# Performance work log

Measured on AMD Instinct MI355X. Metric: run time of the kernel, lower is better.

## Reference

```python
import jax, jax.numpy as jnp
import numpy as np

A1, A2 = 16, 16            # block tile sizes (arr_size1, arr_size2)
G = 1000                   # graph_size (max node index + 1)
EG = 16000                 # number of graph edges (avg degree 16)
SIZE1 = G * A1             # input feature length  (16000)
SIZE2 = G * A2             # output feature length (16000)
NNZ = EG * A1 * A2         # expanded COO entries  (4,096,000)
B = 32                     # batch


def _expand_indices(t0, t1, a1, a2):
    """Vectorized adjust_indices: edge (t0,t1) -> tile of (row,col) pairs.
    row = t0*a2 + j, col = t1*a1 + i  for all i in [a1), j in [a2)."""
    e = t0.shape[0]
    j = np.arange(a2)
    i = np.arange(a1)
    rows = np.broadcast_to(t0[:, None, None] * a2 + j[None, None, :], (e, a1, a2)).reshape(-1)
    cols = np.broadcast_to(t1[:, None, None] * a1 + i[None, :, None], (e, a1, a2)).reshape(-1)
    return rows.astype(np.int32), cols.astype(np.int32)


def setup_inputs() -> dict:
    key = jax.random.key(0)
    ks = jax.random.split(key, 6)
    rng = np.random.default_rng(0)
    t0 = rng.integers(0, G, EG)
    t1 = rng.integers(0, G, EG)
    rows_np, cols_np = _expand_indices(t0, t1, A1, A2)
    # original init: uniform(-1/len(indices), 1/len(indices)) with len([2,nnz])==2 -> U(-0.5, 0.5)
    return {
        "x": jax.random.normal(ks[0], (B, SIZE1, 1), dtype=jnp.float32),
        "weight_mean": jax.random.uniform(ks[1], (NNZ,), jnp.float32, -0.5, 0.5),
        "weight_log_var": jnp.zeros((NNZ,), jnp.float32),
        "b_mean": jax.random.uniform(ks[2], (SIZE2,), jnp.float32, -0.5, 0.5),
        "b_log_var": jnp.zeros((SIZE2,), jnp.float32),
        "eps_w": jax.random.normal(ks[3], (NNZ,), dtype=jnp.float32),
        "eps_b": jax.random.normal(ks[4], (SIZE2,), dtype=jnp.float32),
        "rows": jnp.asarray(rows_np),
        "cols": jnp.asarray(cols_np),
    }


def reference(x, weight_mean, weight_log_var, b_mean, b_log_var, eps_w, eps_b, rows, cols):
    # reparameterization sample of sparse weight values
    values = eps_w * jnp.exp(weight_log_var) + weight_mean          # [NNZ]
    # COO spmm: out[b, r, k] += values[e] * x[b, c, k] for each (r, c) = (rows[e], cols[e])
    contrib = values[None, :, None] * x[:, cols, :]                 # [B, NNZ, 1]
    out = jnp.zeros((x.shape[0], SIZE2, x.shape[2]), x.dtype).at[:, rows, :].add(contrib)
    # reparameterized bias, broadcast over batch
    b = eps_b * jnp.exp(b_log_var) + b_mean                         # [SIZE2]
    out = out + b[None, :, None]
    # kl is explicitly zeroed in the source right before return
    return (out, jnp.asarray(0.0, dtype=x.dtype))
```

## Files before the change

kernel.cpp:

```cpp
#include <hip/hip_runtime.h>

#define EG   16000
#define BB   32
#define SIZE 16000

__global__ __launch_bounds__(256) void init_out_kernel(
    const float* __restrict__ bm, const float* __restrict__ blv,
    const float* __restrict__ eb, float* __restrict__ out)
{
    int r = blockIdx.x * 256 + threadIdx.x;
    int b = blockIdx.y;
    if (r < SIZE) {
        float bias = eb[r] * __expf(blv[r]) + bm[r];
        out[b * SIZE + r] = bias;
    }
    if (blockIdx.x == 0 && blockIdx.y == 0 && threadIdx.x == 0)
        out[BB * SIZE] = 0.0f;
}

__global__ __launch_bounds__(256) void edge_kernel(
    const float* __restrict__ wm, const float* __restrict__ wlv,
    const float* __restrict__ ew, const float* __restrict__ x,
    const int* __restrict__ rows, const int* __restrict__ cols,
    float* __restrict__ out)
{
    __shared__ float vt[256];
    __shared__ float xs[512];

    int e    = blockIdx.x;
    int tid  = threadIdx.x;
    int base = e << 8;

    int t0 = rows[base] >> 4;
    int t1 = cols[base] >> 4;

    vt[tid] = ew[base + tid] * __expf(wlv[base + tid]) + wm[base + tid];

    int j  = tid & 15;
    int b0 = tid >> 4;
    int xb = t1 << 4;
    xs[tid]       = x[ b0        * SIZE + xb + j];
    xs[tid + 256] = x[(b0 + 16)  * SIZE + xb + j];
    __syncthreads();

    float acc0 = 0.f, acc1 = 0.f;
    #pragma unroll
    for (int i = 0; i < 16; ++i) {
        float vv = vt[(i << 4) + j];
        acc0 += vv * xs[((b0)      << 4) + i];
        acc1 += vv * xs[((b0 + 16) << 4) + i];
    }

    int r = (t0 << 4) + j;
    unsafeAtomicAdd(&out[ b0       * SIZE + r], acc0);
    unsafeAtomicAdd(&out[(b0 + 16) * SIZE + r], acc1);
}

extern "C" void kernel_launch(void* const* d_in, const int* in_sizes, int n_in,
                              void* d_out, int out_size, void* d_ws, size_t ws_size,
                              hipStream_t stream) {
    const float* x   = (const float*)d_in[0];
    const float* wm  = (const float*)d_in[1];
    const float* wlv = (const float*)d_in[2];
    const float* bm  = (const float*)d_in[3];
    const float* blv = (const float*)d_in[4];
    const float* ew  = (const float*)d_in[5];
    const float* eb  = (const float*)d_in[6];
    const int* rows  = (const int*)d_in[7];
    const int* cols  = (const int*)d_in[8];
    float* out = (float*)d_out;

    init_out_kernel<<<dim3((SIZE + 255) / 256, BB), 256, 0, stream>>>(bm, blv, eb, out);
    edge_kernel<<<EG, 256, 0, stream>>>(wm, wlv, ew, x, rows, cols, out);
}
```

Before: 137.0 us.

## Process four edges per block with vectorized nontemporal weight loads

Each block now handles four edge tiles instead of one. Weights are read as float4 with nontemporal loads and stored transposed in shared memory so the dot products use vector LDS reads. Launch overhead per block and per-edge index loads are amortized across the four edges, and the atomics per thread rise to eight. The host pointer shuffle is confusing but ends up passing the same arguments as before.

Result: slower. 147.8 us (+7.8%).

```diff
diff --git a/kernel.cpp b/kernel.cpp
--- a/kernel.cpp
+++ b/kernel.cpp
@@ -3,6 +3,8 @@
 #define EG   16000
 #define BB   32
 #define SIZE 16000
+
+typedef float f32x4 __attribute__((ext_vector_type(4)));
 
 __global__ __launch_bounds__(256) void init_out_kernel(
     const float* __restrict__ bm, const float* __restrict__ blv,
@@ -24,36 +26,83 @@
     const int* __restrict__ rows, const int* __restrict__ cols,
     float* __restrict__ out)
 {
-    __shared__ float vt[256];
-    __shared__ float xs[512];
+    __shared__ float vtT[1024];
+    __shared__ float xs[2048];
+    __shared__ int   st0[4];
+    __shared__ int   st1[4];
 
-    int e    = blockIdx.x;
-    int tid  = threadIdx.x;
-    int base = e << 8;
+    int tid = threadIdx.x;
+    int grp = blockIdx.x;
+    int E   = grp << 2;
 
-    int t0 = rows[base] >> 4;
-    int t1 = cols[base] >> 4;
+    if (tid < 8) {
+        int k = tid & 3;
+        if (tid < 4) st1[k] = cols[(long)(E + k) << 8] >> 4;
+        else         st0[k] = rows[(long)(E + k) << 8] >> 4;
+    }
 
-    vt[tid] = ew[base + tid] * __expf(wlv[base + tid]) + wm[base + tid];
+    const f32x4* wm4  = (const f32x4*)wm;
+    const f32x4* wlv4 = (const f32x4*)wlv;
+    const f32x4* ew4  = (const f32x4*)ew;
+    int qi = (grp << 8) + tid;
+    f32x4 m4 = __builtin_nontemporal_load(&wm4[qi]);
+    f32x4 l4 = __builtin_nontemporal_load(&wlv4[qi]);
+    f32x4 e4 = __builtin_nontemporal_load(&ew4[qi]);
+    f32x4 v4;
+    v4.x = e4.x * __expf(l4.x) + m4.x;
+    v4.y = e4.y * __expf(l4.y) + m4.y;
+    v4.z = e4.z * __expf(l4.z) + m4.z;
+    v4.w = e4.w * __expf(l4.w) + m4.w;
+    {
+        int k  = tid >> 6;
+        int i  = (tid >> 2) & 15;
+        int j0 = (tid & 3) << 2;
+        int b  = (k << 8) + i;
+        vtT[b + (j0    ) * 16] = v4.x;
+        vtT[b + (j0 + 1) * 16] = v4.y;
+        vtT[b + (j0 + 2) * 16] = v4.z;
+        vtT[b + (j0 + 3) * 16] = v4.w;
+    }
+    __syncthreads();
+
+    const f32x4* x4 = (const f32x4*)x;
+    f32x4* xs4 = (f32x4*)xs;
+    #pragma unroll
+    for (int h = 0; h < 2; ++h) {
+        int q   = tid + (h << 8);
+        int k   = q >> 7;
+        int rem = q & 127;
+        int b   = rem >> 2;
+        int i4  = rem & 3;
+        xs4[(k << 7) + (b << 2) + i4] =
+            x4[b * (SIZE / 4) + (st1[k] << 2) + i4];
+    }
+    __syncthreads();
 
     int j  = tid & 15;
     int b0 = tid >> 4;
-    int xb = t1 << 4;
-    xs[tid]       = x[ b0        * SIZE + xb + j];
-    xs[tid + 256] = x[(b0 + 16)  * SIZE + xb + j];
-    __syncthreads();
-
-    float acc0 = 0.f, acc1 = 0.f;
+    const f32x4* vtT4 = (const f32x4*)vtT;
+    float acc0[4], acc1[4];
     #pragma unroll
-    for (int i = 0; i < 16; ++i) {
-        float vv = vt[(i << 4) + j];
-        acc0 += vv * xs[((b0)      << 4) + i];
-        acc1 += vv * xs[((b0 + 16) << 4) + i];
+    for (int k = 0; k < 4; ++k) {
+        float a0 = 0.f, a1 = 0.f;
+        #pragma unroll
+        for (int q = 0; q < 4; ++q) {
+            f32x4 w  = vtT4[(k << 6) + (j << 2) + q];
+            f32x4 xa = xs4[(k << 7) + (b0 << 2) + q];
+            f32x4 xb = xs4[(k << 7) + ((b0 + 16) << 2) + q];
+            a0 += w.x * xa.x + w.y * xa.y + w.z * xa.z + w.w * xa.w;
+            a1 += w.x * xb.x + w.y * xb.y + w.z * xb.z + w.w * xb.w;
+        }
+        acc0[k] = a0; acc1[k] = a1;
     }
 
-    int r = (t0 << 4) + j;
-    unsafeAtomicAdd(&out[ b0       * SIZE + r], acc0);
-    unsafeAtomicAdd(&out[(b0 + 16) * SIZE + r], acc1);
+    #pragma unroll
+    for (int k = 0; k < 4; ++k) {
+        int r = (st0[k] << 4) + j;
+        unsafeAtomicAdd(&out[ b0       * SIZE + r], acc0[k]);
+        unsafeAtomicAdd(&out[(b0 + 16) * SIZE + r], acc1[k]);
+    }
 }
 
 extern "C" void kernel_launch(void* const* d_in, const int* in_sizes, int n_in,
@@ -64,12 +113,16 @@
     const float* wlv = (const float*)d_in[2];
     const float* bm  = (const float*)d_in[3];
     const float* blv = (const float*)d_in[4];
-    const float* ew  = (const float*)d_in[5];
-    const float* eb  = (const float*)d_in[6];
-    const int* rows  = (const int*)d_in[7];
-    const int* cols  = (const int*)d_in[8];
+    const float* eb  = (const float*)d_in[5];
+    const int* rows  = (const int*)d_in[6];
+    const int* cols  = (const int*)d_in[7];
+    (void)eb; (void)rows; (void)cols;
+    const float* ew_  = (const float*)d_in[5];
+    const float* eb_  = (const float*)d_in[6];
+    const int* rows_  = (const int*)d_in[7];
+    const int* cols_  = (const int*)d_in[8];
     float* out = (float*)d_out;
 
-    init_out_kernel<<<dim3((SIZE + 255) / 256, BB), 256, 0, stream>>>(bm, blv, eb, out);
-    edge_kernel<<<EG, 256, 0, stream>>>(wm, wlv, ew, x, rows, cols, out);
+    init_out_kernel<<<dim3((SIZE + 255) / 256, BB), 256, 0, stream>>>(bm, blv, eb_, out);
+    edge_kernel<<<EG / 4, 256, 0, stream>>>(wm, wlv, ew_, x, rows_, cols_, out);
 }
```

## Bucket edges by destination node and reduce per node without atomics

Applied to the files above, without the earlier changes.

Adds a bucketing pass that groups edges by destination tile row, then launches one block per output node. Each block accumulates all its incoming edge tiles with double-buffered vectorized loads and writes the result with the fused bias. This removes the global atomic adds and the separate output init kernel, at the cost of an extra memset and bucket pass, a fixed per-node capacity of 64 edges, and possible load imbalance across nodes.

Result: no change. 135.0 us (-1.5%).

```diff
diff --git a/kernel.cpp b/kernel.cpp
--- a/kernel.cpp
+++ b/kernel.cpp
@@ -1,59 +1,143 @@
 #include <hip/hip_runtime.h>
 
 #define EG   16000
+#define NG   1000
 #define BB   32
 #define SIZE 16000
+#define CAP  64
 
-__global__ __launch_bounds__(256) void init_out_kernel(
-    const float* __restrict__ bm, const float* __restrict__ blv,
-    const float* __restrict__ eb, float* __restrict__ out)
+typedef float f32x4 __attribute__((ext_vector_type(4)));
+
+__global__ __launch_bounds__(256) void bucket_kernel(
+    const int* __restrict__ rows, const int* __restrict__ cols,
+    int* __restrict__ cnt, int* __restrict__ bucket)
 {
-    int r = blockIdx.x * 256 + threadIdx.x;
-    int b = blockIdx.y;
-    if (r < SIZE) {
-        float bias = eb[r] * __expf(blv[r]) + bm[r];
-        out[b * SIZE + r] = bias;
+    int e = blockIdx.x * 256 + threadIdx.x;
+    if (e < EG) {
+        int t0 = rows[(long)e << 8] >> 4;
+        int t1 = cols[(long)e << 8] >> 4;
+        int pos = atomicAdd(&cnt[t0], 1);
+        if (pos < CAP) bucket[t0 * CAP + pos] = (e << 10) | t1;
     }
-    if (blockIdx.x == 0 && blockIdx.y == 0 && threadIdx.x == 0)
-        out[BB * SIZE] = 0.0f;
 }
 
-__global__ __launch_bounds__(256) void edge_kernel(
+__global__ __launch_bounds__(256) void spmm_kernel(
     const float* __restrict__ wm, const float* __restrict__ wlv,
     const float* __restrict__ ew, const float* __restrict__ x,
-    const int* __restrict__ rows, const int* __restrict__ cols,
+    const float* __restrict__ bm, const float* __restrict__ blv,
+    const float* __restrict__ eb,
+    const int* __restrict__ cnt, const int* __restrict__ bucket,
     float* __restrict__ out)
 {
-    __shared__ float vt[256];
-    __shared__ float xs[512];
+    __shared__ f32x4 vt[2][4][64];
+    __shared__ f32x4 xs[2][4][160];
+    __shared__ int   sl[CAP];
 
-    int e    = blockIdx.x;
+    int g    = blockIdx.x;
     int tid  = threadIdx.x;
-    int base = e << 8;
+    int wave = tid >> 6;
+    int lane = tid & 63;
+    int jg   = lane & 3;
+    int cb2  = lane >> 2;
 
-    int t0 = rows[base] >> 4;
-    int t1 = cols[base] >> 4;
-
-    vt[tid] = ew[base + tid] * __expf(wlv[base + tid]) + wm[base + tid];
-
-    int j  = tid & 15;
-    int b0 = tid >> 4;
-    int xb = t1 << 4;
-    xs[tid]       = x[ b0        * SIZE + xb + j];
-    xs[tid + 256] = x[(b0 + 16)  * SIZE + xb + j];
+    int n = cnt[g]; n = n < CAP ? n : CAP;
+    if (tid < n) sl[tid] = bucket[g * CAP + tid];
     __syncthreads();
 
-    float acc0 = 0.f, acc1 = 0.f;
-    #pragma unroll
-    for (int i = 0; i < 16; ++i) {
-        float vv = vt[(i << 4) + j];
-        acc0 += vv * xs[((b0)      << 4) + i];
-        acc1 += vv * xs[((b0 + 16) << 4) + i];
+    f32x4 acc0 = {0.f,0.f,0.f,0.f}, acc1 = {0.f,0.f,0.f,0.f};
+    f32x4 m4, l4, g4, xv0, xv1;
+    int iters = (n + 3) >> 2;
+    bool vcur = false, vnxt = false;
+
+    auto issue = [&](int idx) -> bool {
+        bool val = idx < n;
+        if (val) {
+            int pk = sl[idx];
+            int e  = pk >> 10;
+            int t1 = pk & 1023;
+            long wq = ((long)e << 6) + lane;
+            m4 = ((const f32x4*)wm)[wq];
+            l4 = ((const f32x4*)wlv)[wq];
+            g4 = ((const f32x4*)ew)[wq];
+            const f32x4* x4 = (const f32x4*)x;
+            int c0 = lane, c1 = lane + 64;
+            xv0 = x4[(long)(c0 >> 2) * (SIZE/4) + (t1 << 2) + (c0 & 3)];
+            xv1 = x4[(long)(c1 >> 2) * (SIZE/4) + (t1 << 2) + (c1 & 3)];
+        }
+        return val;
+    };
+    auto writeb = [&](int buf, bool val) {
+        if (val) {
+            f32x4 v;
+            v.x = g4.x * __expf(l4.x) + m4.x;
+            v.y = g4.y * __expf(l4.y) + m4.y;
+            v.z = g4.z * __expf(l4.z) + m4.z;
+            v.w = g4.w * __expf(l4.w) + m4.w;
+            vt[buf][wave][lane] = v;
+            int c0 = lane, c1 = lane + 64;
+            xs[buf][wave][(c0 >> 2) * 5 + (c0 & 3)] = xv0;
+            xs[buf][wave][(c1 >> 2) * 5 + (c1 & 3)] = xv1;
+        }
+    };
+    auto compute = [&](int buf, bool val) {
+        if (!val) return;
+        f32x4 a0 = xs[buf][wave][ cb2       * 5 + 0];
+        f32x4 a1 = xs[buf][wave][ cb2       * 5 + 1];
+        f32x4 a2 = xs[buf][wave][ cb2       * 5 + 2];
+        f32x4 a3 = xs[buf][wave][ cb2       * 5 + 3];
+        f32x4 b0 = xs[buf][wave][(cb2 + 16) * 5 + 0];
+        f32x4 b1 = xs[buf][wave][(cb2 + 16) * 5 + 1];
+        f32x4 b2 = xs[buf][wave][(cb2 + 16) * 5 + 2];
+        f32x4 b3 = xs[buf][wave][(cb2 + 16) * 5 + 3];
+        float xra[16] = {a0.x,a0.y,a0.z,a0.w, a1.x,a1.y,a1.z,a1.w,
+                         a2.x,a2.y,a2.z,a2.w, a3.x,a3.y,a3.z,a3.w};
+        float xrb[16] = {b0.x,b0.y,b0.z,b0.w, b1.x,b1.y,b1.z,b1.w,
+                         b2.x,b2.y,b2.z,b2.w, b3.x,b3.y,b3.z,b3.w};
+        #pragma unroll
+        for (int i = 0; i < 16; ++i) {
+            f32x4 w = vt[buf][wave][(i << 2) + jg];
+            acc0 += w * xra[i];
+            acc1 += w * xrb[i];
+        }
+    };
+
+    vcur = issue(wave);
+    writeb(0, vcur);
+    __syncthreads();
+    for (int it = 0; it < iters; ++it) {
+        bool more = (it + 1 < iters);
+        if (more) vnxt = issue(((it + 1) << 2) + wave);
+        compute(it & 1, vcur);
+        if (more) writeb((it + 1) & 1, vnxt);
+        __syncthreads();
+        vcur = vnxt;
     }
 
-    int r = (t0 << 4) + j;
-    unsafeAtomicAdd(&out[ b0       * SIZE + r], acc0);
-    unsafeAtomicAdd(&out[(b0 + 16) * SIZE + r], acc1);
+    f32x4* sred = &xs[0][0][0];
+    sred[(wave << 7) + (lane << 1) + 0] = acc0;
+    sred[(wave << 7) + (lane << 1) + 1] = acc1;
+    __syncthreads();
+    if (tid < 128) {
+        int cb  = tid >> 2;
+        int jgf = tid & 3;
+        int h   = cb >> 4;
+        int sl_ = ((cb & 15) << 2) + jgf;
+        f32x4 s = sred[(0 << 7) + (sl_ << 1) + h]
+                + sred[(1 << 7) + (sl_ << 1) + h]
+                + sred[(2 << 7) + (sl_ << 1) + h]
+                + sred[(3 << 7) + (sl_ << 1) + h];
+        int r0 = (g << 4) + (jgf << 2);
+        f32x4 b4 = *(const f32x4*)&bm[r0];
+        f32x4 v4 = *(const f32x4*)&blv[r0];
+        f32x4 e4 = *(const f32x4*)&eb[r0];
+        f32x4 o;
+        o.x = s.x + (e4.x * __expf(v4.x) + b4.x);
+        o.y = s.y + (e4.y * __expf(v4.y) + b4.y);
+        o.z = s.z + (e4.z * __expf(v4.z) + b4.z);
+        o.w = s.w + (e4.w * __expf(v4.w) + b4.w);
+        *(f32x4*)&out[(long)cb * SIZE + r0] = o;
+    }
+    if (g == 0 && tid == 0) out[(long)BB * SIZE] = 0.0f;
 }
 
 extern "C" void kernel_launch(void* const* d_in, const int* in_sizes, int n_in,
@@ -70,6 +154,12 @@
     const int* cols  = (const int*)d_in[8];
     float* out = (float*)d_out;
 
-    init_out_kernel<<<dim3((SIZE + 255) / 256, BB), 256, 0, stream>>>(bm, blv, eb, out);
-    edge_kernel<<<EG, 256, 0, stream>>>(wm, wlv, ew, x, rows, cols, out);
+    char* ws = (char*)d_ws;
+    int* cnt    = (int*)(ws);
+    int* bucket = (int*)(ws + 4096);
+
+    hipMemsetAsync(cnt, 0, 4096, stream);
+    bucket_kernel<<<(EG + 255) / 256, 256, 0, stream>>>(rows, cols, cnt, bucket);
+    spmm_kernel<<<NG, 256, 0, stream>>>(wm, wlv, ew, x, bm, blv, eb,
+                                        cnt, bucket, out);
 }
```
